# Kernel tuning notes

Measured on AMD Instinct MI355X. Metric: run time of the kernel, lower is better.

## Reference

```python
import jax, jax.numpy as jnp
import numpy as np

B, S, D = 4, 2048, 1024  # batch, seq_len, d_emb (even for Givens pairs)


def givens_rotate(r, x):
    """Apply 2x2 Givens block rotations defined by r [D] to x [..., D]."""
    g = r.reshape(-1, 2)
    g = g / jnp.linalg.norm(g, axis=-1, keepdims=True)  # normalize (cos, sin) pairs
    xp = x.reshape(x.shape[:-1] + (x.shape[-1] // 2, 2))
    c, s = g[:, 0], g[:, 1]
    y0 = c * xp[..., 0] - s * xp[..., 1]
    y1 = c * xp[..., 1] + s * xp[..., 0]
    return jnp.stack([y0, y1], axis=-1).reshape(x.shape)


def setup_inputs() -> dict:
    key = jax.random.key(0)
    k1, k2 = jax.random.split(key, 2)
    Q = jax.random.normal(k1, (B, S, D), dtype=jnp.float32)
    # QKV_rotation.weight ~ U(-1, 1) per original init (before the identity overwrite)
    rot_w = jax.random.uniform(k2, (3, D), dtype=jnp.float32, minval=-1.0, maxval=1.0)
    scale = jnp.array([np.sqrt(D)], dtype=jnp.float32)
    bias = jnp.zeros((), dtype=jnp.float32)
    return {"Q": Q, "rot_w": rot_w, "scale": scale, "bias": bias}


def reference(Q, rot_w, scale, bias):
    # Givens-rotation 'projections' for q/k/v
    q = givens_rotate(rot_w[0], Q)
    k = givens_rotate(rot_w[1], Q)
    v = givens_rotate(rot_w[2], Q)
    # prepend zero time coordinate -> points on the Lorentz model ambient space
    zeros = jnp.zeros(Q.shape[:-1] + (1,), Q.dtype)
    q = jnp.concatenate([zeros, q], axis=-1)[:, None]  # [B,1,S,D+1]
    k = jnp.concatenate([zeros, k], axis=-1)[:, None]
    v = jnp.concatenate([zeros, v], axis=-1)[:, None]
    # Lorentz signature (-, +, +, ...)
    sgn = jnp.concatenate([-jnp.ones((1,), Q.dtype), jnp.ones((q.shape[-1] - 1,), Q.dtype)])
    # cinner(q, k): time-negated inner product -> scores [B,1,S,S]
    cin = jnp.einsum('bhqd,bhkd->bhqk', q * sgn, k)
    attn = jax.nn.softmax((2.0 + 2.0 * cin) / scale + bias, axis=-1)
    # Lorentz mid-point: weighted sum normalized by sqrt(|<m,m>_L|)
    ave = jnp.einsum('bhqk,bhkd->bhqd', attn, v)
    inner = jnp.sum(ave * ave * sgn, axis=-1, keepdims=True)
    denom = jnp.sqrt(jnp.clip(jnp.abs(inner), 1e-8, None))
    out = (ave / denom)[:, 0]  # [B,S,D+1]
    return out[..., 1:]  # drop time coordinate -> [B,S,D]
```

## Files before the change

### kernel.cpp

```cpp
#include <hip/hip_runtime.h>

typedef _Float16 h16;
typedef _Float16 half8 __attribute__((ext_vector_type(8)));
typedef _Float16 half4v __attribute__((ext_vector_type(4)));
typedef float floatx4 __attribute__((ext_vector_type(4)));

static constexpr int Bb_ = 4, S_ = 2048, D_ = 1024;

static __device__ __forceinline__ void gl_lds16(const void* g, void* l) {
  __builtin_amdgcn_global_load_lds(
      (const __attribute__((address_space(1))) unsigned int*)g,
      (__attribute__((address_space(3))) unsigned int*)l, 16, 0, 0);
}

__global__ __launch_bounds__(256) void k_prep_t(const float* __restrict__ Q,
                                                const float* __restrict__ rot,
                                                h16* __restrict__ Qh,
                                                h16* __restrict__ Kh,
                                                h16* __restrict__ VhT) {
  __shared__ __align__(16) h16 tile[64][64];
  int d0 = blockIdx.x * 64, s0 = blockIdx.y * 64, b = blockIdx.z;
  int t = threadIdx.x;
  const float* Qb = Q + ((size_t)b * S_ + s0) * D_ + d0;
  h16* Qhb = Qh + ((size_t)b * S_ + s0) * D_ + d0;
  h16* Khb = Kh + ((size_t)b * S_ + s0) * D_ + d0;
#pragma unroll
  for (int i = 0; i < 4; ++i) {
    int c = t + 256 * i;
    int row = c >> 4;
    int col = (c & 15) * 4;
    float4 q = *(const float4*)&Qb[(size_t)row * D_ + col];
    int dg = (d0 + col) >> 2;
    float4 r0 = ((const float4*)rot)[dg];
    float4 r1 = ((const float4*)rot)[D_ / 4 + dg];
    float4 r2 = ((const float4*)rot)[2 * D_ / 4 + dg];
    float nq0 = r0.x * r0.x + r0.y * r0.y;
    float nk0 = r1.x * r1.x + r1.y * r1.y;
    float iqk0 = rsqrtf(nq0 * nk0);
    float cc0 = (r0.x * r1.x + r0.y * r1.y) * iqk0;
    float ss0 = (r0.x * r1.y - r0.y * r1.x) * iqk0;
    float y0 = cc0 * q.x - ss0 * q.y;
    float y1 = cc0 * q.y + ss0 * q.x;
    float nq1 = r0.z * r0.z + r0.w * r0.w;
    float nk1 = r1.z * r1.z + r1.w * r1.w;
    float iqk1 = rsqrtf(nq1 * nk1);
    float cc1 = (r0.z * r1.z + r0.w * r1.w) * iqk1;
    float ss1 = (r0.z * r1.w - r0.w * r1.z) * iqk1;
    float y2 = cc1 * q.z - ss1 * q.w;
    float y3 = cc1 * q.w + ss1 * q.z;
    float inv0 = rsqrtf(r2.x * r2.x + r2.y * r2.y);
    float cv0 = r2.x * inv0, sv0 = r2.y * inv0;
    float v0 = cv0 * q.x - sv0 * q.y;
    float v1 = cv0 * q.y + sv0 * q.x;
    float inv1 = rsqrtf(r2.z * r2.z + r2.w * r2.w);
    float cv1 = r2.z * inv1, sv1 = r2.w * inv1;
    float v2 = cv1 * q.z - sv1 * q.w;
    float v3 = cv1 * q.w + sv1 * q.z;
    half4v kh = {(h16)y0, (h16)y1, (h16)y2, (h16)y3};
    half4v qh = {(h16)q.x, (h16)q.y, (h16)q.z, (h16)q.w};
    half4v vh = {(h16)v0, (h16)v1, (h16)v2, (h16)v3};
    *(half4v*)&Qhb[(size_t)row * D_ + col] = qh;
    *(half4v*)&Khb[(size_t)row * D_ + col] = kh;
    int pcol = col ^ ((row >> 3) << 3);
    *(half4v*)&tile[row][pcol] = vh;
  }
  __syncthreads();
  h16* dst = VhT + ((size_t)b * D_ + d0) * S_ + s0;
#pragma unroll
  for (int i = 0; i < 2; ++i) {
    int c = t + 256 * i;
    int drow = c >> 3;
    int sc = (c & 7) * 8;
    int xr = sc;
    half8 v;
#pragma unroll
    for (int j = 0; j < 8; ++j) v[j] = tile[sc + j][drow ^ xr];
    *(half8*)&dst[(size_t)drow * S_ + sc] = v;
  }
}

#define G_FENCE asm volatile("" ::: "memory")
#define G_BAR                     \
  do {                            \
    G_FENCE;                      \
    __builtin_amdgcn_s_barrier(); \
    G_FENCE;                      \
  } while (0)

template <int NF, bool OUT16>
__global__ __launch_bounds__(512, 2) void k_gemm8(
    const char* __restrict__ A, int a_pitch, unsigned long long a_batch,
    const char* __restrict__ Bt, int b_pitch, unsigned long long b_batch,
    void* __restrict__ C, int c_pitch, unsigned long long c_batch, int Kdim,
    const float* __restrict__ scale_p) {
  constexpr int BNR = NF * 64;
  constexpr int JQ = NF / 2;
  __shared__ __align__(16) h16 As[2][2][256 * 32];
  __shared__ __align__(16) h16 Bs[2][2][BNR * 32];
  const int t = threadIdx.x;
  const int lane = t & 63;
  const int w = t >> 6;
  const int wm = (w >> 2) * 128;
  const int wn = (w & 3) * (NF * 16);
  const int id = blockIdx.x + 8 * (blockIdx.y + 8 * blockIdx.z);
  const int L = (id & 7) * 32 + (id >> 3);
  const int tm = L & 7, tn = (L >> 3) & 7, tz = L >> 6;
  const char* Ab = A + (unsigned long long)tz * a_batch +
                   (unsigned long long)(tm * 256) * (unsigned long long)a_pitch;
  const char* Bb = Bt + (unsigned long long)tz * b_batch +
                   (unsigned long long)(tn * BNR) * (unsigned long long)b_pitch;
  const int srow = t >> 2;
  const int scol = ((t & 3) ^ ((t >> 3) & 3)) << 4;
  const int lds_o = t * 16;
  const int mrow = lane & 15, kc = lane >> 4;
  const int koff = (kc ^ ((mrow >> 1) & 3)) << 3;
  const int NT = Kdim >> 6;

#define SG_A(bf, kt, hm)                                                  \
  do {                                                                    \
    const char* sp_ = Ab +                                                \
                      (unsigned long long)(srow + (hm) * 128) * a_pitch + \
                      (kt) * 128 + scol;                                  \
    gl_lds16(sp_, (char*)&As[bf][0][(hm) * 128 * 32] + lds_o);            \
    gl_lds16(sp_ + 64, (char*)&As[bf][1][(hm) * 128 * 32] + lds_o);       \
  } while (0)
#define SG_B(bf, kt, hm)                                                  \
  do {                                                                    \
    const char* sp_ = Bb +                                                \
                      (unsigned long long)(srow + (hm) * 128) * b_pitch + \
                      (kt) * 128 + scol;                                  \
    gl_lds16(sp_, (char*)&Bs[bf][0][(hm) * 128 * 32] + lds_o);            \
    gl_lds16(sp_ + 64, (char*)&Bs[bf][1][(hm) * 128 * 32] + lds_o);       \
  } while (0)

  half8 ar0[4][2], ar1[4][2], br0[JQ][2], br1[JQ][2];
  floatx4 acc[8][NF];
#pragma unroll
  for (int i = 0; i < 8; ++i)
#pragma unroll
    for (int j = 0; j < NF; ++j) acc[i][j] = (floatx4){0.f, 0.f, 0.f, 0.f};

#define LDA_(bf, mh, DST)                                                \
  do {                                                                   \
    _Pragma("unroll") for (int i_ = 0; i_ < 4; ++i_) {                   \
      DST[i_][0] = *(const half8*)&As[bf][0]                             \
                       [(wm + ((mh) * 4 + i_) * 16 + mrow) * 32 + koff]; \
      DST[i_][1] = *(const half8*)&As[bf][1]                             \
                       [(wm + ((mh) * 4 + i_) * 16 + mrow) * 32 + koff]; \
    }                                                                    \
  } while (0)
#define LDB_(bf, nh, DST)                                                \
  do {                                                                   \
    _Pragma("unroll") for (int j_ = 0; j_ < JQ; ++j_) {                  \
      DST[j_][0] = *(const half8*)&Bs[bf][0]                             \
                       [(wn + ((nh)*JQ + j_) * 16 + mrow) * 32 + koff];  \
      DST[j_][1] = *(const half8*)&Bs[bf][1]                             \
                       [(wn + ((nh)*JQ + j_) * 16 + mrow) * 32 + koff];  \
    }                                                                    \
  } while (0)
#define QUAD(mh, nh, AF, BF)                                                 \
  do {                                                                       \
    __builtin_amdgcn_s_setprio(1);                                           \
    _Pragma("unroll") for (int i_ = 0; i_ < 4; ++i_)                         \
        _Pragma("unroll") for (int j_ = 0; j_ < JQ; ++j_) {                  \
      acc[(mh) * 4 + i_][(nh)*JQ + j_] =                                     \
          __builtin_amdgcn_mfma_f32_16x16x32_f16(                            \
              AF[i_][0], BF[j_][0], acc[(mh) * 4 + i_][(nh)*JQ + j_], 0, 0,  \
              0);                                                            \
      acc[(mh) * 4 + i_][(nh)*JQ + j_] =                                     \
          __builtin_amdgcn_mfma_f32_16x16x32_f16(                            \
              AF[i_][1], BF[j_][1], acc[(mh) * 4 + i_][(nh)*JQ + j_], 0, 0,  \
              0);                                                            \
    }                                                                        \
    __builtin_amdgcn_s_setprio(0);                                           \
  } while (0)

  SG_A(0, 0, 0);
  SG_A(0, 0, 1);
  SG_B(0, 0, 0);
  if constexpr (NF == 4) SG_B(0, 0, 1);
  SG_B(1, 1, 0);
  if constexpr (NF == 4) SG_B(1, 1, 1);
  SG_A(1, 1, 0);
  if constexpr (NF == 4)
    asm volatile("s_waitcnt vmcnt(6)" ::: "memory");
  else
    asm volatile("s_waitcnt vmcnt(4)" ::: "memory");
  G_BAR;
  LDA_(0, 0, ar0);
  LDB_(0, 0, br0);

#define TILE_(bf, nb, u)                                   \
  do {                                                     \
    const int k1_ = ((u) + 1 < NT) ? (u) + 1 : NT - 1;     \
    const int k2_ = ((u) + 2 < NT) ? (u) + 2 : NT - 1;     \
                                                   \
    SG_A(nb, k1_, 1);                                      \
    G_BAR;                                                 \
    LDB_(bf, 1, br1);                                      \
    QUAD(0, 0, ar0, br0);                                  \
                                                   \
    G_BAR;                                                 \
    LDA_(bf, 1, ar1);                                      \
    QUAD(0, 1, ar0, br1);                                  \
                                                   \
    SG_B(bf, k2_, 0);                                      \
    G_BAR;                                                 \
    QUAD(1, 0, ar1, br0);                                  \
                                                   \
    if constexpr (NF == 4) SG_B(bf, k2_, 1);               \
    SG_A(bf, k2_, 0);                                      \
    if constexpr (NF == 4)                                 \
      asm volatile("s_waitcnt vmcnt(6)" ::: "memory");     \
    else                                                   \
      asm volatile("s_waitcnt vmcnt(4)" ::: "memory");     \
    G_BAR;                                                 \
    LDA_(nb, 0, ar0);  \
    LDB_(nb, 0, br0);                                      \
    QUAD(1, 1, ar1, br1);                                  \
  } while (0)

  for (int u = 0; u < NT; u += 2) {
    TILE_(0, 1, u);
    TILE_(1, 0, u + 1);
  }
  asm volatile("s_waitcnt vmcnt(0)" ::: "memory");

  const int m0 = tm * 256 + wm;
  const int n0 = tn * BNR + wn;
  const int ccol = lane & 15;
  const int rq = (lane >> 4) * 4;
  if constexpr (OUT16) {
    const float aexp = 2.0f / scale_p[0];
    h16* Cb = (h16*)C + (unsigned long long)tz * c_batch;
#pragma unroll
    for (int i = 0; i < 8; ++i)
#pragma unroll
      for (int j = 0; j < NF; ++j)
#pragma unroll
        for (int r = 0; r < 4; ++r)
          Cb[(unsigned long long)(m0 + i * 16 + rq + r) * c_pitch +
             (n0 + j * 16 + ccol)] = (h16)__expf(acc[i][j][r] * aexp - 8.0f);
  } else {
    float* Cb = (float*)C + (unsigned long long)tz * c_batch;
#pragma unroll
    for (int i = 0; i < 8; ++i)
#pragma unroll
      for (int j = 0; j < NF; ++j)
#pragma unroll
        for (int r = 0; r < 4; ++r)
          Cb[(unsigned long long)(m0 + i * 16 + rq + r) * c_pitch +
             (n0 + j * 16 + ccol)] = acc[i][j][r];
  }
#undef TILE_
#undef QUAD
#undef LDB_
#undef LDA_
#undef SG_B
#undef SG_A
}

__global__ __launch_bounds__(256) void k_epilogue(float* __restrict__ O) {
  int wv = threadIdx.x >> 6, ln = threadIdx.x & 63;
  int row = blockIdx.x * 4 + wv;
  float* base = O + (size_t)row * D_;
  float4 u[4];
#pragma unroll
  for (int r = 0; r < 4; ++r) u[r] = ((const float4*)base)[ln + 64 * r];
  float ss = 0.f;
#pragma unroll
  for (int r = 0; r < 4; ++r)
    ss += u[r].x * u[r].x + u[r].y * u[r].y + u[r].z * u[r].z + u[r].w * u[r].w;
#pragma unroll
  for (int off = 32; off; off >>= 1) ss += __shfl_xor(ss, off);
  float f = rsqrtf(fmaxf(ss, 1e-30f));
#pragma unroll
  for (int r = 0; r < 4; ++r) {
    float4 o;
    o.x = u[r].x * f;
    o.y = u[r].y * f;
    o.z = u[r].z * f;
    o.w = u[r].w * f;
    ((float4*)base)[ln + 64 * r] = o;
  }
}

extern "C" void kernel_launch(void* const* d_in, const int* in_sizes, int n_in,
                              void* d_out, int out_size, void* d_ws, size_t ws_size,
                              hipStream_t stream) {
  const float* Q = (const float*)d_in[0];
  const float* rot = (const float*)d_in[1];
  const float* scale = (const float*)d_in[2];
  float* O = (float*)d_out;
  char* ws = (char*)d_ws;
  const size_t MB = 1024ull * 1024ull;
  h16* Qh = (h16*)(ws);
  h16* Kh = (h16*)(ws + 16 * MB);
  h16* VhT = (h16*)(ws + 32 * MB);
  h16* Sl = (h16*)(ws + 48 * MB);

  k_prep_t<<<dim3(D_ / 64, S_ / 64, Bb_), 256, 0, stream>>>(Q, rot, Qh, Kh, VhT);
  k_gemm8<4, true><<<dim3(8, 8, 4), 512, 0, stream>>>(
      (const char*)Qh, D_ * 2, (unsigned long long)S_ * D_ * 2,
      (const char*)Kh, D_ * 2, (unsigned long long)S_ * D_ * 2,
      (void*)Sl, S_, (unsigned long long)S_ * S_, D_, scale);
  k_gemm8<2, false><<<dim3(8, 8, 4), 512, 0, stream>>>(
      (const char*)Sl, S_ * 2, (unsigned long long)S_ * S_ * 2,
      (const char*)VhT, S_ * 2, (unsigned long long)D_ * S_ * 2,
      (void*)O, D_, (unsigned long long)S_ * D_, S_, nullptr);
  k_epilogue<<<dim3(Bb_ * S_ / 4), 256, 0, stream>>>(O);
}
```

Before: 181.0 us.

## Fuse row-norm epilogue into second GEMM via cross-block flag synchronization

Removes the separate epilogue kernel by computing per-row squared-norm partials inside the P·V GEMM. Each block publishes its 256-row partials to a workspace buffer, then spins on a per-row-group atomic counter until all 8 column blocks have arrived. It then sums the partials and writes the normalized output directly. This saves one full read-modify-write pass over the fp32 output and one kernel launch. In exchange it relies on all 8 blocks of a group being co-resident (the grid is 256 blocks at 2 per CU, so this should fit) and adds spin-wait latency.

```diff
diff --git a/kernel.cpp b/kernel.cpp
--- a/kernel.cpp
+++ b/kernel.cpp
@@ -17,10 +17,13 @@
                                                 const float* __restrict__ rot,
                                                 h16* __restrict__ Qh,
                                                 h16* __restrict__ Kh,
-                                                h16* __restrict__ VhT) {
+                                                h16* __restrict__ VhT,
+                                                unsigned int* __restrict__ flags) {
   __shared__ __align__(16) h16 tile[64][64];
   int d0 = blockIdx.x * 64, s0 = blockIdx.y * 64, b = blockIdx.z;
   int t = threadIdx.x;
+  if (flags && blockIdx.x == 0 && blockIdx.y == 0 && blockIdx.z == 0 && t < 32)
+    flags[t] = 0u;
   const float* Qb = Q + ((size_t)b * S_ + s0) * D_ + d0;
   h16* Qhb = Qh + ((size_t)b * S_ + s0) * D_ + d0;
   h16* Khb = Kh + ((size_t)b * S_ + s0) * D_ + d0;
@@ -92,7 +95,8 @@
     const char* __restrict__ A, int a_pitch, unsigned long long a_batch,
     const char* __restrict__ Bt, int b_pitch, unsigned long long b_batch,
     void* __restrict__ C, int c_pitch, unsigned long long c_batch, int Kdim,
-    const float* __restrict__ scale_p) {
+    const float* __restrict__ scale_p, float* __restrict__ pss,
+    unsigned int* __restrict__ flags) {
   constexpr int BNR = NF * 64;
   constexpr int JQ = NF / 2;
   __shared__ __align__(16) h16 As[2][2][256 * 32];
@@ -243,14 +247,74 @@
              (n0 + j * 16 + ccol)] = (h16)__expf(acc[i][j][r] * aexp - 8.0f);
   } else {
     float* Cb = (float*)C + (unsigned long long)tz * c_batch;
-#pragma unroll
-    for (int i = 0; i < 8; ++i)
-#pragma unroll
-      for (int j = 0; j < NF; ++j)
-#pragma unroll
-        for (int r = 0; r < 4; ++r)
-          Cb[(unsigned long long)(m0 + i * 16 + rq + r) * c_pitch +
-             (n0 + j * 16 + ccol)] = acc[i][j][r];
+    if (pss) {
+      const int grp = tz * 8 + tm;
+      __syncthreads();
+      float* wsum = (float*)&As[0][0][0];
+      float* finv = wsum + 4 * 256;
+      float part[8][4];
+#pragma unroll
+      for (int i = 0; i < 8; ++i)
+#pragma unroll
+        for (int r = 0; r < 4; ++r) {
+          float s = acc[i][0][r] * acc[i][0][r];
+          if constexpr (NF > 1) s += acc[i][1][r] * acc[i][1][r];
+#pragma unroll
+          for (int m = 1; m < 16; m <<= 1) s += __shfl_xor(s, m);
+          part[i][r] = s;
+        }
+      if ((lane & 15) == 0) {
+#pragma unroll
+        for (int i = 0; i < 8; ++i)
+#pragma unroll
+          for (int r = 0; r < 4; ++r)
+            wsum[(w & 3) * 256 + wm + i * 16 + rq + r] = part[i][r];
+      }
+      __syncthreads();
+      if (t < 256) {
+        float s = wsum[t] + wsum[256 + t] + wsum[512 + t] + wsum[768 + t];
+        __hip_atomic_store(&pss[((unsigned)grp * 8 + tn) * 256 + t], s,
+                           __ATOMIC_RELAXED, __HIP_MEMORY_SCOPE_AGENT);
+      }
+      __syncthreads();
+      if (t == 0) {
+        __hip_atomic_fetch_add(&flags[grp], 1u, __ATOMIC_ACQ_REL,
+                               __HIP_MEMORY_SCOPE_AGENT);
+        while (__hip_atomic_load(&flags[grp], __ATOMIC_ACQUIRE,
+                                 __HIP_MEMORY_SCOPE_AGENT) < 8u)
+          __builtin_amdgcn_s_sleep(2);
+      }
+      __syncthreads();
+      if (t < 256) {
+        float ss2 = 0.f;
+#pragma unroll
+        for (int c = 0; c < 8; ++c)
+          ss2 += __hip_atomic_load(&pss[((unsigned)grp * 8 + c) * 256 + t],
+                                   __ATOMIC_RELAXED, __HIP_MEMORY_SCOPE_AGENT);
+        finv[t] = rsqrtf(fmaxf(ss2, 1e-30f));
+      }
+      __syncthreads();
+#pragma unroll
+      for (int i = 0; i < 8; ++i) {
+#pragma unroll
+        for (int r = 0; r < 4; ++r) {
+          const float f = finv[wm + i * 16 + rq + r];
+#pragma unroll
+          for (int j = 0; j < NF; ++j)
+            Cb[(unsigned long long)(m0 + i * 16 + rq + r) * c_pitch +
+               (n0 + j * 16 + ccol)] = acc[i][j][r] * f;
+        }
+      }
+    } else {
+#pragma unroll
+      for (int i = 0; i < 8; ++i)
+#pragma unroll
+        for (int j = 0; j < NF; ++j)
+#pragma unroll
+          for (int r = 0; r < 4; ++r)
+            Cb[(unsigned long long)(m0 + i * 16 + rq + r) * c_pitch +
+               (n0 + j * 16 + ccol)] = acc[i][j][r];
+    }
   }
 #undef TILE_
 #undef QUAD
@@ -298,15 +362,23 @@
   h16* Kh = (h16*)(ws + 16 * MB);
   h16* VhT = (h16*)(ws + 32 * MB);
   h16* Sl = (h16*)(ws + 48 * MB);
-
-  k_prep_t<<<dim3(D_ / 64, S_ / 64, Bb_), 256, 0, stream>>>(Q, rot, Qh, Kh, VhT);
+  float* pss = (float*)(ws + 80 * MB);
+  unsigned int* flags = (unsigned int*)(ws + 80 * MB + 256 * 1024);
+  const bool fused = ws_size >= 80 * MB + 256 * 1024 + 128;
+  if (!fused) {
+    pss = nullptr;
+    flags = nullptr;
+  }
+
+  k_prep_t<<<dim3(D_ / 64, S_ / 64, Bb_), 256, 0, stream>>>(Q, rot, Qh, Kh,
+                                                            VhT, flags);
   k_gemm8<4, true><<<dim3(8, 8, 4), 512, 0, stream>>>(
       (const char*)Qh, D_ * 2, (unsigned long long)S_ * D_ * 2,
       (const char*)Kh, D_ * 2, (unsigned long long)S_ * D_ * 2,
-      (void*)Sl, S_, (unsigned long long)S_ * S_, D_, scale);
+      (void*)Sl, S_, (unsigned long long)S_ * S_, D_, scale, nullptr, nullptr);
   k_gemm8<2, false><<<dim3(8, 8, 4), 512, 0, stream>>>(
       (const char*)Sl, S_ * 2, (unsigned long long)S_ * S_ * 2,
       (const char*)VhT, S_ * 2, (unsigned long long)D_ * S_ * 2,
-      (void*)O, D_, (unsigned long long)S_ * D_, S_, nullptr);
-  k_epilogue<<<dim3(Bb_ * S_ / 4), 256, 0, stream>>>(O);
-}
+      (void*)O, D_, (unsigned long long)S_ * D_, S_, nullptr, pss, flags);
+  if (!fused) k_epilogue<<<dim3(Bb_ * S_ / 4), 256, 0, stream>>>(O);
+}
```

After: 178.0 us. Within noise of the previous version (-1.7%).
